# Kernel optimization log

Measured on AMD Instinct MI355X. Metric: run time of the kernel, lower is better.

## Reference

```python
import jax, jax.numpy as jnp
import numpy as np

N_NODES = 100000

def _sage_conv(x, src, dst, W_l, b_l, W_r):
    # PyG SAGEConv(aggr='mean'): out = lin_l(mean_{j in N(i)} x_j) + lin_r(x_i)
    agg = jax.ops.segment_sum(x[src], dst, num_segments=N_NODES)          # [N, F]
    cnt = jax.ops.segment_sum(jnp.ones_like(dst, dtype=x.dtype), dst,
                              num_segments=N_NODES)                        # [N]
    mean = agg / jnp.maximum(cnt, 1.0)[:, None]
    return mean @ W_l + b_l + x @ W_r

def setup_inputs() -> dict:
    key = jax.random.key(0)
    ks = jax.random.split(key, 10)
    F_in, H = 128, 16
    E, P = 1600000, 2000000
    x = jax.random.normal(ks[0], (N_NODES, F_in), dtype=jnp.float32)
    edge_index = jax.random.randint(ks[1], (2, E), 0, N_NODES, dtype=jnp.int64)
    decode_index = jax.random.randint(ks[2], (2, P), 0, N_NODES, dtype=jnp.int64)
    s1 = 1.0 / np.sqrt(F_in)
    s2 = 1.0 / np.sqrt(H)
    W1l = jax.random.uniform(ks[3], (F_in, H), jnp.float32, -s1, s1)
    b1 = jax.random.uniform(ks[4], (H,), jnp.float32, -s1, s1)
    W1r = jax.random.uniform(ks[5], (F_in, H), jnp.float32, -s1, s1)
    W2l = jax.random.uniform(ks[6], (H, H), jnp.float32, -s2, s2)
    b2 = jax.random.uniform(ks[7], (H,), jnp.float32, -s2, s2)
    W2r = jax.random.uniform(ks[8], (H, H), jnp.float32, -s2, s2)
    return {"x": x, "W1l": W1l, "b1": b1, "W1r": W1r,
            "W2l": W2l, "b2": b2, "W2r": W2r,
            "edge_index": edge_index, "decode_index": decode_index}

def reference(x, W1l, b1, W1r, W2l, b2, W2r, edge_index, decode_index):
    src, dst = edge_index[0], edge_index[1]
    h = _sage_conv(x, src, dst, W1l, b1, W1r)          # conv1
    h = jax.nn.relu(h)                                  # relu (dropout: eval -> identity)
    h = _sage_conv(h, src, dst, W2l, b2, W2r)           # conv2
    logits = jnp.sum(h[decode_index[0]] * h[decode_index[1]], axis=1)  # [P]
    return jax.nn.sigmoid(logits)
```

## Files before the change

### kernel.cpp

```cpp
#include <hip/hip_runtime.h>
#include <hip/hip_fp16.h>

#define N_NODES 100000
#define F_IN 128
#define H 16
#define NBIN 391
#define BINCAP 4608
#define ECHUNK 8192
#define QSCALE 4096.0f
#define QINV (1.0f / 4096.0f)

__device__ inline unsigned int packi16(float a, float b) {
  int ia = __float2int_rn(fminf(fmaxf(a * QSCALE, -32767.f), 32767.f));
  int ib = __float2int_rn(fminf(fmaxf(b * QSCALE, -32767.f), 32767.f));
  return (unsigned int)((ia & 0xffff) | (ib << 16));
}

__global__ void __launch_bounds__(512) k_init(int* __restrict__ binCur) {
  int t = threadIdx.x;
  if (t < NBIN) binCur[t] = t * BINCAP;
}

__global__ void __launch_bounds__(256) k_lin1(
    const float* __restrict__ x, const float* __restrict__ W1l,
    const float* __restrict__ W1r, unsigned short* __restrict__ y1l,
    float* __restrict__ y1r) {
  __shared__ float red[3 * 32 * 64];
  int t = threadIdx.x;
  int part = __builtin_amdgcn_readfirstlane(t >> 6);
  int ln = t & 63;
  int n = blockIdx.x * 64 + ln;
  int nc = (n < N_NODES) ? n : (N_NODES - 1);
  const float4* xr = (const float4*)(x + (size_t)nc * F_IN + part * (F_IN / 4));
  float4 xv[8];
#pragma unroll
  for (int j = 0; j < 8; ++j) xv[j] = xr[j];
  const float* Wl = W1l + part * (F_IN / 4) * H;
  const float* Wr = W1r + part * (F_IN / 4) * H;
  float al[H], ar[H];
#pragma unroll
  for (int c = 0; c < H; ++c) { al[c] = 0.f; ar[c] = 0.f; }
#pragma unroll
  for (int j = 0; j < 8; ++j) {
    float xs[4] = {xv[j].x, xv[j].y, xv[j].z, xv[j].w};
#pragma unroll
    for (int jj = 0; jj < 4; ++jj) {
      int k = j * 4 + jj;
#pragma unroll
      for (int c = 0; c < H; ++c) {
        al[c] = fmaf(xs[jj], Wl[k * H + c], al[c]);
        ar[c] = fmaf(xs[jj], Wr[k * H + c], ar[c]);
      }
    }
  }
  if (part != 0) {
    int base = (part - 1) * 2048;
#pragma unroll
    for (int c = 0; c < H; ++c) {
      red[base + c * 64 + ln] = al[c];
      red[base + (H + c) * 64 + ln] = ar[c];
    }
  }
  __syncthreads();
  if (part == 0 && n < N_NODES) {
#pragma unroll
    for (int c = 0; c < H; ++c) {
      al[c] = ((al[c] + red[c * 64 + ln]) + red[2048 + c * 64 + ln])
              + red[4096 + c * 64 + ln];
      ar[c] = ((ar[c] + red[(H + c) * 64 + ln]) + red[2048 + (H + c) * 64 + ln])
              + red[4096 + (H + c) * 64 + ln];
    }
    uint4 w0, w1;
    w0.x = packi16(al[0], al[1]);  w0.y = packi16(al[2], al[3]);
    w0.z = packi16(al[4], al[5]);  w0.w = packi16(al[6], al[7]);
    w1.x = packi16(al[8], al[9]);  w1.y = packi16(al[10], al[11]);
    w1.z = packi16(al[12], al[13]); w1.w = packi16(al[14], al[15]);
    uint4* ol = (uint4*)(y1l + (size_t)n * H);
    ol[0] = w0;
    ol[1] = w1;
    float4* orr = (float4*)(y1r + (size_t)n * H);
#pragma unroll
    for (int q = 0; q < 4; ++q)
      orr[q] = make_float4(ar[4 * q], ar[4 * q + 1], ar[4 * q + 2], ar[4 * q + 3]);
  }
}

__global__ void __launch_bounds__(512) k_binfill(
    const int* __restrict__ src, const int* __restrict__ dst,
    int* __restrict__ binCur, int* __restrict__ recs, int E) {
  __shared__ int hist[512];
  __shared__ int gbase[512];
  __shared__ int cnt2[512];
  int t = threadIdx.x;
  hist[t] = 0;
  cnt2[t] = 0;
  __syncthreads();
  int base = blockIdx.x * ECHUNK;
  int rec[16], bin[16];
#pragma unroll
  for (int j = 0; j < 16; ++j) {
    int e = base + j * 512 + t;
    if (e < E) {
      int s = src[e];
      int d = dst[e];
      rec[j] = (s << 8) | (d & 255);
      bin[j] = d >> 8;
      atomicAdd(&hist[bin[j]], 1);
    } else {
      bin[j] = -1;
    }
  }
  __syncthreads();
  if (t < NBIN) {
    int c = hist[t];
    gbase[t] = (c > 0) ? atomicAdd(&binCur[t], c) : 0;
  }
  __syncthreads();
#pragma unroll
  for (int j = 0; j < 16; ++j) {
    if (bin[j] >= 0) {
      int loc = atomicAdd(&cnt2[bin[j]], 1);
      int slot = gbase[bin[j]] + loc;
      if (slot < (bin[j] + 1) * BINCAP)
        recs[slot] = rec[j];
    }
  }
}

__global__ void __launch_bounds__(512) k_group(
    int* __restrict__ recs, const int* __restrict__ binCur,
    int* __restrict__ deg, int* __restrict__ rowBeg) {
  __shared__ int lrec[BINCAP];
  __shared__ int hist[256];
  __shared__ int off[256];
  __shared__ int cur[256];
  int t = threadIdx.x;
  int b = blockIdx.x;
  int rbase = b * BINCAP;
  int R = binCur[b] - rbase;
  if (R > BINCAP) R = BINCAP;
  if (t < 256) hist[t] = 0;
  __syncthreads();
#pragma unroll
  for (int j = 0; j < 9; ++j) {
    int idx = j * 512 + t;
    if (idx < R) {
      int r = recs[rbase + idx];
      lrec[idx] = r;
      atomicAdd(&hist[r & 255], 1);
    }
  }
  __syncthreads();
  if (t < 256) off[t] = hist[t];
  __syncthreads();
  for (int o = 1; o < 256; o <<= 1) {
    int u = 0;
    if (t < 256 && t >= o) u = off[t - o];
    __syncthreads();
    if (t < 256) off[t] += u;
    __syncthreads();
  }
  if (t < 256) {
    int ex = off[t] - hist[t];
    cur[t] = ex;
    int n = (b << 8) + t;
    if (n < N_NODES) {
      deg[n] = hist[t];
      rowBeg[n] = rbase + ex;
    }
  }
  __syncthreads();
#pragma unroll
  for (int j = 0; j < 9; ++j) {
    int idx = j * 512 + t;
    if (idx < R) {
      int r = lrec[idx];
      int slot = atomicAdd(&cur[r & 255], 1);
      recs[rbase + slot] = r >> 8;
    }
  }
}

__global__ void __launch_bounds__(256) k_gather1(
    const int* __restrict__ srcSorted, const int* __restrict__ deg,
    const int* __restrict__ rowBeg, const unsigned short* __restrict__ y1l,
    const float* __restrict__ y1r, const float* __restrict__ b1,
    const float* __restrict__ W2l, const float* __restrict__ W2r,
    unsigned short* __restrict__ z2l, float* __restrict__ z2r) {
  int tid = blockIdx.x * 256 + threadIdx.x;
  int n = tid >> 2;
  int q = tid & 3;
  if (n >= N_NODES) return;
  int beg = rowBeg[n];
  int dg = deg[n];
  int end = beg + dg;
  int acc0 = 0, acc1 = 0, acc2 = 0, acc3 = 0;
  int i = beg;
  for (; i + 8 <= end; i += 8) {
    int sqa = srcSorted[i + q];
    int sqb = srcSorted[i + 4 + q];
#pragma unroll
    for (int j = 0; j < 4; ++j) {
      int sa = __shfl(sqa, j, 4);
      int sb = __shfl(sqb, j, 4);
      uint2 va = *(const uint2*)(y1l + (size_t)sa * H + q * 4);
      uint2 vb = *(const uint2*)(y1l + (size_t)sb * H + q * 4);
      acc0 += (((int)(va.x << 16)) >> 16) + (((int)(vb.x << 16)) >> 16);
      acc1 += (((int)va.x) >> 16) + (((int)vb.x) >> 16);
      acc2 += (((int)(va.y << 16)) >> 16) + (((int)(vb.y << 16)) >> 16);
      acc3 += (((int)va.y) >> 16) + (((int)vb.y) >> 16);
    }
  }
  for (; i + 4 <= end; i += 4) {
    int sq = srcSorted[i + q];
#pragma unroll
    for (int j = 0; j < 4; ++j) {
      int sj = __shfl(sq, j, 4);
      uint2 v = *(const uint2*)(y1l + (size_t)sj * H + q * 4);
      acc0 += ((int)(v.x << 16)) >> 16;
      acc1 += ((int)v.x) >> 16;
      acc2 += ((int)(v.y << 16)) >> 16;
      acc3 += ((int)v.y) >> 16;
    }
  }
  for (; i < end; ++i) {
    int sj = srcSorted[i];
    uint2 v = *(const uint2*)(y1l + (size_t)sj * H + q * 4);
    acc0 += ((int)(v.x << 16)) >> 16;
    acc1 += ((int)v.x) >> 16;
    acc2 += ((int)(v.y << 16)) >> 16;
    acc3 += ((int)v.y) >> 16;
  }
  float s = (1.f / fmaxf((float)dg, 1.f)) * QINV;
  float4 yr = *(const float4*)(y1r + (size_t)n * H + q * 4);
  float4 bb = *(const float4*)(b1 + q * 4);
  float h1x = fmaxf(fmaf((float)acc0, s, bb.x + yr.x), 0.f);
  float h1y = fmaxf(fmaf((float)acc1, s, bb.y + yr.y), 0.f);
  float h1z = fmaxf(fmaf((float)acc2, s, bb.z + yr.z), 0.f);
  float h1w = fmaxf(fmaf((float)acc3, s, bb.w + yr.w), 0.f);
  float zl0 = 0.f, zl1 = 0.f, zl2 = 0.f, zl3 = 0.f;
  float zr0 = 0.f, zr1 = 0.f, zr2 = 0.f, zr3 = 0.f;
#pragma unroll
  for (int sl = 0; sl < 4; ++sl) {
    float hx = __shfl(h1x, sl, 4);
    float hy = __shfl(h1y, sl, 4);
    float hz = __shfl(h1z, sl, 4);
    float hw = __shfl(h1w, sl, 4);
    float hk4[4] = {hx, hy, hz, hw};
#pragma unroll
    for (int j = 0; j < 4; ++j) {
      int k = sl * 4 + j;
      float4 wl = *(const float4*)(W2l + k * H + q * 4);
      float4 wr = *(const float4*)(W2r + k * H + q * 4);
      float hk = hk4[j];
      zl0 = fmaf(hk, wl.x, zl0); zl1 = fmaf(hk, wl.y, zl1);
      zl2 = fmaf(hk, wl.z, zl2); zl3 = fmaf(hk, wl.w, zl3);
      zr0 = fmaf(hk, wr.x, zr0); zr1 = fmaf(hk, wr.y, zr1);
      zr2 = fmaf(hk, wr.z, zr2); zr3 = fmaf(hk, wr.w, zr3);
    }
  }
  uint2 pk;
  pk.x = packi16(zl0, zl1);
  pk.y = packi16(zl2, zl3);
  *(uint2*)(z2l + (size_t)n * H + q * 4) = pk;
  *(float4*)(z2r + (size_t)n * H + q * 4) = make_float4(zr0, zr1, zr2, zr3);
}

__global__ void __launch_bounds__(256) k_gather2(
    const int* __restrict__ srcSorted, const int* __restrict__ deg,
    const int* __restrict__ rowBeg, const unsigned short* __restrict__ z2l,
    const float* __restrict__ z2r, const float* __restrict__ b2,
    __half* __restrict__ h2) {
  int tid = blockIdx.x * 256 + threadIdx.x;
  int n = tid >> 2;
  int q = tid & 3;
  if (n >= N_NODES) return;
  int beg = rowBeg[n];
  int dg = deg[n];
  int end = beg + dg;
  int acc0 = 0, acc1 = 0, acc2 = 0, acc3 = 0;
  int i = beg;
  for (; i + 8 <= end; i += 8) {
    int sqa = srcSorted[i + q];
    int sqb = srcSorted[i + 4 + q];
#pragma unroll
    for (int j = 0; j < 4; ++j) {
      int sa = __shfl(sqa, j, 4);
      int sb = __shfl(sqb, j, 4);
      uint2 va = *(const uint2*)(z2l + (size_t)sa * H + q * 4);
      uint2 vb = *(const uint2*)(z2l + (size_t)sb * H + q * 4);
      acc0 += (((int)(va.x << 16)) >> 16) + (((int)(vb.x << 16)) >> 16);
      acc1 += (((int)va.x) >> 16) + (((int)vb.x) >> 16);
      acc2 += (((int)(va.y << 16)) >> 16) + (((int)(vb.y << 16)) >> 16);
      acc3 += (((int)va.y) >> 16) + (((int)vb.y) >> 16);
    }
  }
  for (; i + 4 <= end; i += 4) {
    int sq = srcSorted[i + q];
#pragma unroll
    for (int j = 0; j < 4; ++j) {
      int sj = __shfl(sq, j, 4);
      uint2 v = *(const uint2*)(z2l + (size_t)sj * H + q * 4);
      acc0 += ((int)(v.x << 16)) >> 16;
      acc1 += ((int)v.x) >> 16;
      acc2 += ((int)(v.y << 16)) >> 16;
      acc3 += ((int)v.y) >> 16;
    }
  }
  for (; i < end; ++i) {
    int sj = srcSorted[i];
    uint2 v = *(const uint2*)(z2l + (size_t)sj * H + q * 4);
    acc0 += ((int)(v.x << 16)) >> 16;
    acc1 += ((int)v.x) >> 16;
    acc2 += ((int)(v.y << 16)) >> 16;
    acc3 += ((int)v.y) >> 16;
  }
  float s = (1.f / fmaxf((float)dg, 1.f)) * QINV;
  float4 zr = *(const float4*)(z2r + (size_t)n * H + q * 4);
  float4 bb = *(const float4*)(b2 + q * 4);
  float v0 = fmaf((float)acc0, s, bb.x + zr.x);
  float v1 = fmaf((float)acc1, s, bb.y + zr.y);
  float v2 = fmaf((float)acc2, s, bb.z + zr.z);
  float v3 = fmaf((float)acc3, s, bb.w + zr.w);
  __half2 h0 = __floats2half2_rn(v0, v1);
  __half2 h1 = __floats2half2_rn(v2, v3);
  uint2 pk;
  pk.x = *(unsigned int*)&h0;
  pk.y = *(unsigned int*)&h1;
  *(uint2*)(h2 + (size_t)n * H + q * 4) = pk;
}

__device__ inline float dot8h(uint4 u, uint4 v) {
  float acc = 0.f;
  const unsigned int* uw = (const unsigned int*)&u;
  const unsigned int* vw = (const unsigned int*)&v;
#pragma unroll
  for (int j = 0; j < 4; ++j) {
    float2 a = __half22float2(*(const __half2*)&uw[j]);
    float2 b = __half22float2(*(const __half2*)&vw[j]);
    acc = fmaf(a.x, b.x, acc);
    acc = fmaf(a.y, b.y, acc);
  }
  return acc;
}

__global__ void __launch_bounds__(256) k_decode(
    const int* __restrict__ ps, const int* __restrict__ pd,
    const __half* __restrict__ h2, float* __restrict__ out, int P) {
  int t = blockIdx.x * 256 + threadIdx.x;
  int p = t * 2;
  if (p >= P) return;
  int2 av = *(const int2*)(ps + p);
  int2 bv = *(const int2*)(pd + p);
  const uint4* ha0 = (const uint4*)(h2 + (size_t)av.x * H);
  const uint4* hb0 = (const uint4*)(h2 + (size_t)bv.x * H);
  const uint4* ha1 = (const uint4*)(h2 + (size_t)av.y * H);
  const uint4* hb1 = (const uint4*)(h2 + (size_t)bv.y * H);
  uint4 u00 = ha0[0], u01 = ha0[1];
  uint4 v00 = hb0[0], v01 = hb0[1];
  uint4 u10 = ha1[0], u11 = ha1[1];
  uint4 v10 = hb1[0], v11 = hb1[1];
  float d0 = dot8h(u00, v00) + dot8h(u01, v01);
  float d1 = dot8h(u10, v10) + dot8h(u11, v11);
  float o0 = 1.f / (1.f + __expf(-d0));
  float o1 = 1.f / (1.f + __expf(-d1));
  if (p + 1 < P) {
    *(float2*)(out + p) = make_float2(o0, o1);
  } else {
    out[p] = o0;
  }
}

extern "C" void kernel_launch(void* const* d_in, const int* in_sizes, int n_in,
                              void* d_out, int out_size, void* d_ws, size_t ws_size,
                              hipStream_t stream) {
  const float* x   = (const float*)d_in[0];
  const float* W1l = (const float*)d_in[1];
  const float* b1  = (const float*)d_in[2];
  const float* W1r = (const float*)d_in[3];
  const float* W2l = (const float*)d_in[4];
  const float* b2  = (const float*)d_in[5];
  const float* W2r = (const float*)d_in[6];
  const int* ei = (const int*)d_in[7];
  const int* di = (const int*)d_in[8];
  const int E = in_sizes[7] / 2;
  const int P = in_sizes[8] / 2;

  const size_t NF = (size_t)N_NODES * H;
  unsigned short* y1l = (unsigned short*)d_ws;
  __half*         h2  = (__half*)y1l;
  unsigned short* z2l = y1l + NF;
  float*  y1r = (float*)(z2l + NF);
  float*  z2r = y1r;
  int* recs   = (int*)(y1r + NF);
  int* binCur = recs + (size_t)NBIN * BINCAP;
  int* deg    = binCur + 512;
  int* rowBeg = deg + N_NODES;

  const int lin1Blocks = (N_NODES + 63) / 64;
  const int fillBlocks = (E + ECHUNK - 1) / ECHUNK;
  const int gatherBlocks = ((N_NODES * 4) + 255) / 256;
  const int decodeBlocks = ((P + 1) / 2 + 255) / 256;

  k_init<<<1, 512, 0, stream>>>(binCur);
  k_lin1<<<lin1Blocks, 256, 0, stream>>>(x, W1l, W1r, y1l, y1r);
  k_binfill<<<fillBlocks, 512, 0, stream>>>(ei, ei + E, binCur, recs, E);
  k_group<<<NBIN, 512, 0, stream>>>(recs, binCur, deg, rowBeg);
  k_gather1<<<gatherBlocks, 256, 0, stream>>>(recs, deg, rowBeg, y1l, y1r,
                                              b1, W2l, W2r, z2l, z2r);
  k_gather2<<<gatherBlocks, 256, 0, stream>>>(recs, deg, rowBeg, z2l, z2r,
                                              b2, h2);
  k_decode<<<decodeBlocks, 256, 0, stream>>>(di, di + P, h2, (float*)d_out, P);
}
```

Before: 214.6 us.

## Replace CSR grouping and gathers with per-bin shared-memory atomic aggregation

Drops the k_group sorting pass and the per-node CSR gather kernels. Each 256-node bin block now reads its unsorted edge records directly, gathers the 16-channel quantized source rows and accumulates them with LDS integer atomics, then applies the epilogue (mean, bias, relu, second-layer matmul). This removes one kernel launch, the deg/rowBeg arrays and the recs rewrite pass. In exchange there is heavy LDS atomic contention and only 391 blocks, which may underfill the GPU.

```diff
diff --git a/kernel.cpp b/kernel.cpp
--- a/kernel.cpp
+++ b/kernel.cpp
@@ -9,6 +9,9 @@
 #define ECHUNK 8192
 #define QSCALE 4096.0f
 #define QINV (1.0f / 4096.0f)
+
+#define SXL(u) (((int)((u) << 16)) >> 16)
+#define SXH(u) (((int)(u)) >> 16)
 
 __device__ inline unsigned int packi16(float a, float b) {
   int ia = __float2int_rn(fminf(fmaxf(a * QSCALE, -32767.f), 32767.f));
@@ -127,207 +130,178 @@
   }
 }
 
-__global__ void __launch_bounds__(512) k_group(
-    int* __restrict__ recs, const int* __restrict__ binCur,
-    int* __restrict__ deg, int* __restrict__ rowBeg) {
-  __shared__ int lrec[BINCAP];
-  __shared__ int hist[256];
-  __shared__ int off[256];
-  __shared__ int cur[256];
+__global__ void __launch_bounds__(512) k_agg1(
+    const int* __restrict__ recs, const int* __restrict__ binCur,
+    const unsigned short* __restrict__ y1l, const float* __restrict__ y1r,
+    const float* __restrict__ b1, const float* __restrict__ W2l,
+    const float* __restrict__ W2r, unsigned short* __restrict__ z2l,
+    float* __restrict__ z2r) {
+  __shared__ int acc[16][256];
+  __shared__ int cnt[256];
+  __shared__ float hf[16][256];
+  __shared__ float w2l[256];
+  __shared__ float w2r[256];
   int t = threadIdx.x;
   int b = blockIdx.x;
+#pragma unroll
+  for (int j = 0; j < 8; ++j) ((int*)acc)[j * 512 + t] = 0;
+  if (t < 256) { cnt[t] = 0; w2l[t] = W2l[t]; }
+  else         w2r[t - 256] = W2r[t - 256];
+  __syncthreads();
   int rbase = b * BINCAP;
   int R = binCur[b] - rbase;
   if (R > BINCAP) R = BINCAP;
-  if (t < 256) hist[t] = 0;
-  __syncthreads();
+  int rr[9];
 #pragma unroll
   for (int j = 0; j < 9; ++j) {
     int idx = j * 512 + t;
-    if (idx < R) {
-      int r = recs[rbase + idx];
-      lrec[idx] = r;
-      atomicAdd(&hist[r & 255], 1);
-    }
-  }
-  __syncthreads();
-  if (t < 256) off[t] = hist[t];
-  __syncthreads();
-  for (int o = 1; o < 256; o <<= 1) {
-    int u = 0;
-    if (t < 256 && t >= o) u = off[t - o];
-    __syncthreads();
-    if (t < 256) off[t] += u;
-    __syncthreads();
-  }
-  if (t < 256) {
-    int ex = off[t] - hist[t];
-    cur[t] = ex;
-    int n = (b << 8) + t;
-    if (n < N_NODES) {
-      deg[n] = hist[t];
-      rowBeg[n] = rbase + ex;
-    }
-  }
-  __syncthreads();
+    rr[j] = (idx < R) ? recs[rbase + idx] : -1;
+  }
+  uint4 va[9], vb[9];
+#pragma unroll
+  for (int j = 0; j < 9; ++j) {
+    int s = (rr[j] >= 0) ? (rr[j] >> 8) : 0;
+    const uint4* yp = (const uint4*)(y1l + (size_t)s * H);
+    va[j] = yp[0];
+    vb[j] = yp[1];
+  }
+#pragma unroll
+  for (int j = 0; j < 9; ++j) {
+    if (rr[j] >= 0) {
+      int nb = rr[j] & 255;
+      uint4 v0 = va[j], v1 = vb[j];
+      atomicAdd(&cnt[nb], 1);
+      atomicAdd(&acc[0][nb],  SXL(v0.x)); atomicAdd(&acc[1][nb],  SXH(v0.x));
+      atomicAdd(&acc[2][nb],  SXL(v0.y)); atomicAdd(&acc[3][nb],  SXH(v0.y));
+      atomicAdd(&acc[4][nb],  SXL(v0.z)); atomicAdd(&acc[5][nb],  SXH(v0.z));
+      atomicAdd(&acc[6][nb],  SXL(v0.w)); atomicAdd(&acc[7][nb],  SXH(v0.w));
+      atomicAdd(&acc[8][nb],  SXL(v1.x)); atomicAdd(&acc[9][nb],  SXH(v1.x));
+      atomicAdd(&acc[10][nb], SXL(v1.y)); atomicAdd(&acc[11][nb], SXH(v1.y));
+      atomicAdd(&acc[12][nb], SXL(v1.z)); atomicAdd(&acc[13][nb], SXH(v1.z));
+      atomicAdd(&acc[14][nb], SXL(v1.w)); atomicAdd(&acc[15][nb], SXH(v1.w));
+    }
+  }
+  __syncthreads();
+  int node = t >> 1;
+  int half = t & 1;
+  int coff = half * 8;
+  int n = (b << 8) + node;
+  if (n < N_NODES) {
+    float s = QINV / fmaxf((float)cnt[node], 1.f);
+    const float4* yrp = (const float4*)(y1r + (size_t)n * H + coff);
+    float4 y0 = yrp[0], y1v = yrp[1];
+    const float4* bp = (const float4*)(b1 + coff);
+    float4 b0 = bp[0], b1v = bp[1];
+    float yv[8] = {y0.x, y0.y, y0.z, y0.w, y1v.x, y1v.y, y1v.z, y1v.w};
+    float bv[8] = {b0.x, b0.y, b0.z, b0.w, b1v.x, b1v.y, b1v.z, b1v.w};
+#pragma unroll
+    for (int c = 0; c < 8; ++c) {
+      float h = fmaf((float)acc[coff + c][node], s, bv[c] + yv[c]);
+      hf[coff + c][node] = fmaxf(h, 0.f);
+    }
+  } else {
+#pragma unroll
+    for (int c = 0; c < 8; ++c) hf[coff + c][node] = 0.f;
+  }
+  __syncthreads();
+  float zl[8], zr[8];
+#pragma unroll
+  for (int c = 0; c < 8; ++c) { zl[c] = 0.f; zr[c] = 0.f; }
+#pragma unroll
+  for (int k = 0; k < 16; ++k) {
+    float hk = hf[k][node];
+#pragma unroll
+    for (int c = 0; c < 8; ++c) {
+      zl[c] = fmaf(hk, w2l[k * 16 + coff + c], zl[c]);
+      zr[c] = fmaf(hk, w2r[k * 16 + coff + c], zr[c]);
+    }
+  }
+  if (n < N_NODES) {
+    uint4 pk;
+    pk.x = packi16(zl[0], zl[1]);
+    pk.y = packi16(zl[2], zl[3]);
+    pk.z = packi16(zl[4], zl[5]);
+    pk.w = packi16(zl[6], zl[7]);
+    *(uint4*)(z2l + (size_t)n * H + coff) = pk;
+    float4* zp = (float4*)(z2r + (size_t)n * H + coff);
+    zp[0] = make_float4(zr[0], zr[1], zr[2], zr[3]);
+    zp[1] = make_float4(zr[4], zr[5], zr[6], zr[7]);
+  }
+}
+
+__global__ void __launch_bounds__(512) k_agg2(
+    const int* __restrict__ recs, const int* __restrict__ binCur,
+    const unsigned short* __restrict__ z2l, const float* __restrict__ z2r,
+    const float* __restrict__ b2, __half* __restrict__ h2) {
+  __shared__ int acc[16][256];
+  __shared__ int cnt[256];
+  int t = threadIdx.x;
+  int b = blockIdx.x;
+#pragma unroll
+  for (int j = 0; j < 8; ++j) ((int*)acc)[j * 512 + t] = 0;
+  if (t < 256) cnt[t] = 0;
+  __syncthreads();
+  int rbase = b * BINCAP;
+  int R = binCur[b] - rbase;
+  if (R > BINCAP) R = BINCAP;
+  int rr[9];
 #pragma unroll
   for (int j = 0; j < 9; ++j) {
     int idx = j * 512 + t;
-    if (idx < R) {
-      int r = lrec[idx];
-      int slot = atomicAdd(&cur[r & 255], 1);
-      recs[rbase + slot] = r >> 8;
-    }
-  }
-}
-
-__global__ void __launch_bounds__(256) k_gather1(
-    const int* __restrict__ srcSorted, const int* __restrict__ deg,
-    const int* __restrict__ rowBeg, const unsigned short* __restrict__ y1l,
-    const float* __restrict__ y1r, const float* __restrict__ b1,
-    const float* __restrict__ W2l, const float* __restrict__ W2r,
-    unsigned short* __restrict__ z2l, float* __restrict__ z2r) {
-  int tid = blockIdx.x * 256 + threadIdx.x;
-  int n = tid >> 2;
-  int q = tid & 3;
-  if (n >= N_NODES) return;
-  int beg = rowBeg[n];
-  int dg = deg[n];
-  int end = beg + dg;
-  int acc0 = 0, acc1 = 0, acc2 = 0, acc3 = 0;
-  int i = beg;
-  for (; i + 8 <= end; i += 8) {
-    int sqa = srcSorted[i + q];
-    int sqb = srcSorted[i + 4 + q];
-#pragma unroll
-    for (int j = 0; j < 4; ++j) {
-      int sa = __shfl(sqa, j, 4);
-      int sb = __shfl(sqb, j, 4);
-      uint2 va = *(const uint2*)(y1l + (size_t)sa * H + q * 4);
-      uint2 vb = *(const uint2*)(y1l + (size_t)sb * H + q * 4);
-      acc0 += (((int)(va.x << 16)) >> 16) + (((int)(vb.x << 16)) >> 16);
-      acc1 += (((int)va.x) >> 16) + (((int)vb.x) >> 16);
-      acc2 += (((int)(va.y << 16)) >> 16) + (((int)(vb.y << 16)) >> 16);
-      acc3 += (((int)va.y) >> 16) + (((int)vb.y) >> 16);
-    }
-  }
-  for (; i + 4 <= end; i += 4) {
-    int sq = srcSorted[i + q];
-#pragma unroll
-    for (int j = 0; j < 4; ++j) {
-      int sj = __shfl(sq, j, 4);
-      uint2 v = *(const uint2*)(y1l + (size_t)sj * H + q * 4);
-      acc0 += ((int)(v.x << 16)) >> 16;
-      acc1 += ((int)v.x) >> 16;
-      acc2 += ((int)(v.y << 16)) >> 16;
-      acc3 += ((int)v.y) >> 16;
-    }
-  }
-  for (; i < end; ++i) {
-    int sj = srcSorted[i];
-    uint2 v = *(const uint2*)(y1l + (size_t)sj * H + q * 4);
-    acc0 += ((int)(v.x << 16)) >> 16;
-    acc1 += ((int)v.x) >> 16;
-    acc2 += ((int)(v.y << 16)) >> 16;
-    acc3 += ((int)v.y) >> 16;
-  }
-  float s = (1.f / fmaxf((float)dg, 1.f)) * QINV;
-  float4 yr = *(const float4*)(y1r + (size_t)n * H + q * 4);
-  float4 bb = *(const float4*)(b1 + q * 4);
-  float h1x = fmaxf(fmaf((float)acc0, s, bb.x + yr.x), 0.f);
-  float h1y = fmaxf(fmaf((float)acc1, s, bb.y + yr.y), 0.f);
-  float h1z = fmaxf(fmaf((float)acc2, s, bb.z + yr.z), 0.f);
-  float h1w = fmaxf(fmaf((float)acc3, s, bb.w + yr.w), 0.f);
-  float zl0 = 0.f, zl1 = 0.f, zl2 = 0.f, zl3 = 0.f;
-  float zr0 = 0.f, zr1 = 0.f, zr2 = 0.f, zr3 = 0.f;
-#pragma unroll
-  for (int sl = 0; sl < 4; ++sl) {
-    float hx = __shfl(h1x, sl, 4);
-    float hy = __shfl(h1y, sl, 4);
-    float hz = __shfl(h1z, sl, 4);
-    float hw = __shfl(h1w, sl, 4);
-    float hk4[4] = {hx, hy, hz, hw};
-#pragma unroll
-    for (int j = 0; j < 4; ++j) {
-      int k = sl * 4 + j;
-      float4 wl = *(const float4*)(W2l + k * H + q * 4);
-      float4 wr = *(const float4*)(W2r + k * H + q * 4);
-      float hk = hk4[j];
-      zl0 = fmaf(hk, wl.x, zl0); zl1 = fmaf(hk, wl.y, zl1);
-      zl2 = fmaf(hk, wl.z, zl2); zl3 = fmaf(hk, wl.w, zl3);
-      zr0 = fmaf(hk, wr.x, zr0); zr1 = fmaf(hk, wr.y, zr1);
-      zr2 = fmaf(hk, wr.z, zr2); zr3 = fmaf(hk, wr.w, zr3);
-    }
-  }
-  uint2 pk;
-  pk.x = packi16(zl0, zl1);
-  pk.y = packi16(zl2, zl3);
-  *(uint2*)(z2l + (size_t)n * H + q * 4) = pk;
-  *(float4*)(z2r + (size_t)n * H + q * 4) = make_float4(zr0, zr1, zr2, zr3);
-}
-
-__global__ void __launch_bounds__(256) k_gather2(
-    const int* __restrict__ srcSorted, const int* __restrict__ deg,
-    const int* __restrict__ rowBeg, const unsigned short* __restrict__ z2l,
-    const float* __restrict__ z2r, const float* __restrict__ b2,
-    __half* __restrict__ h2) {
-  int tid = blockIdx.x * 256 + threadIdx.x;
-  int n = tid >> 2;
-  int q = tid & 3;
-  if (n >= N_NODES) return;
-  int beg = rowBeg[n];
-  int dg = deg[n];
-  int end = beg + dg;
-  int acc0 = 0, acc1 = 0, acc2 = 0, acc3 = 0;
-  int i = beg;
-  for (; i + 8 <= end; i += 8) {
-    int sqa = srcSorted[i + q];
-    int sqb = srcSorted[i + 4 + q];
-#pragma unroll
-    for (int j = 0; j < 4; ++j) {
-      int sa = __shfl(sqa, j, 4);
-      int sb = __shfl(sqb, j, 4);
-      uint2 va = *(const uint2*)(z2l + (size_t)sa * H + q * 4);
-      uint2 vb = *(const uint2*)(z2l + (size_t)sb * H + q * 4);
-      acc0 += (((int)(va.x << 16)) >> 16) + (((int)(vb.x << 16)) >> 16);
-      acc1 += (((int)va.x) >> 16) + (((int)vb.x) >> 16);
-      acc2 += (((int)(va.y << 16)) >> 16) + (((int)(vb.y << 16)) >> 16);
-      acc3 += (((int)va.y) >> 16) + (((int)vb.y) >> 16);
-    }
-  }
-  for (; i + 4 <= end; i += 4) {
-    int sq = srcSorted[i + q];
-#pragma unroll
-    for (int j = 0; j < 4; ++j) {
-      int sj = __shfl(sq, j, 4);
-      uint2 v = *(const uint2*)(z2l + (size_t)sj * H + q * 4);
-      acc0 += ((int)(v.x << 16)) >> 16;
-      acc1 += ((int)v.x) >> 16;
-      acc2 += ((int)(v.y << 16)) >> 16;
-      acc3 += ((int)v.y) >> 16;
-    }
-  }
-  for (; i < end; ++i) {
-    int sj = srcSorted[i];
-    uint2 v = *(const uint2*)(z2l + (size_t)sj * H + q * 4);
-    acc0 += ((int)(v.x << 16)) >> 16;
-    acc1 += ((int)v.x) >> 16;
-    acc2 += ((int)(v.y << 16)) >> 16;
-    acc3 += ((int)v.y) >> 16;
-  }
-  float s = (1.f / fmaxf((float)dg, 1.f)) * QINV;
-  float4 zr = *(const float4*)(z2r + (size_t)n * H + q * 4);
-  float4 bb = *(const float4*)(b2 + q * 4);
-  float v0 = fmaf((float)acc0, s, bb.x + zr.x);
-  float v1 = fmaf((float)acc1, s, bb.y + zr.y);
-  float v2 = fmaf((float)acc2, s, bb.z + zr.z);
-  float v3 = fmaf((float)acc3, s, bb.w + zr.w);
-  __half2 h0 = __floats2half2_rn(v0, v1);
-  __half2 h1 = __floats2half2_rn(v2, v3);
-  uint2 pk;
-  pk.x = *(unsigned int*)&h0;
-  pk.y = *(unsigned int*)&h1;
-  *(uint2*)(h2 + (size_t)n * H + q * 4) = pk;
+    rr[j] = (idx < R) ? recs[rbase + idx] : -1;
+  }
+  uint4 va[9], vb[9];
+#pragma unroll
+  for (int j = 0; j < 9; ++j) {
+    int s = (rr[j] >= 0) ? (rr[j] >> 8) : 0;
+    const uint4* yp = (const uint4*)(z2l + (size_t)s * H);
+    va[j] = yp[0];
+    vb[j] = yp[1];
+  }
+#pragma unroll
+  for (int j = 0; j < 9; ++j) {
+    if (rr[j] >= 0) {
+      int nb = rr[j] & 255;
+      uint4 v0 = va[j], v1 = vb[j];
+      atomicAdd(&cnt[nb], 1);
+      atomicAdd(&acc[0][nb],  SXL(v0.x)); atomicAdd(&acc[1][nb],  SXH(v0.x));
+      atomicAdd(&acc[2][nb],  SXL(v0.y)); atomicAdd(&acc[3][nb],  SXH(v0.y));
+      atomicAdd(&acc[4][nb],  SXL(v0.z)); atomicAdd(&acc[5][nb],  SXH(v0.z));
+      atomicAdd(&acc[6][nb],  SXL(v0.w)); atomicAdd(&acc[7][nb],  SXH(v0.w));
+      atomicAdd(&acc[8][nb],  SXL(v1.x)); atomicAdd(&acc[9][nb],  SXH(v1.x));
+      atomicAdd(&acc[10][nb], SXL(v1.y)); atomicAdd(&acc[11][nb], SXH(v1.y));
+      atomicAdd(&acc[12][nb], SXL(v1.z)); atomicAdd(&acc[13][nb], SXH(v1.z));
+      atomicAdd(&acc[14][nb], SXL(v1.w)); atomicAdd(&acc[15][nb], SXH(v1.w));
+    }
+  }
+  __syncthreads();
+  int node = t >> 1;
+  int half = t & 1;
+  int coff = half * 8;
+  int n = (b << 8) + node;
+  if (n < N_NODES) {
+    float s = QINV / fmaxf((float)cnt[node], 1.f);
+    const float4* zrp = (const float4*)(z2r + (size_t)n * H + coff);
+    float4 z0 = zrp[0], z1 = zrp[1];
+    const float4* bp = (const float4*)(b2 + coff);
+    float4 b0 = bp[0], b1v = bp[1];
+    float zv[8] = {z0.x, z0.y, z0.z, z0.w, z1.x, z1.y, z1.z, z1.w};
+    float bv[8] = {b0.x, b0.y, b0.z, b0.w, b1v.x, b1v.y, b1v.z, b1v.w};
+    float v[8];
+#pragma unroll
+    for (int c = 0; c < 8; ++c)
+      v[c] = fmaf((float)acc[coff + c][node], s, bv[c] + zv[c]);
+    __half2 h0 = __floats2half2_rn(v[0], v[1]);
+    __half2 h1 = __floats2half2_rn(v[2], v[3]);
+    __half2 h2p = __floats2half2_rn(v[4], v[5]);
+    __half2 h3 = __floats2half2_rn(v[6], v[7]);
+    uint4 pk;
+    pk.x = *(unsigned int*)&h0;
+    pk.y = *(unsigned int*)&h1;
+    pk.z = *(unsigned int*)&h2p;
+    pk.w = *(unsigned int*)&h3;
+    *(uint4*)(h2 + (size_t)n * H + coff) = pk;
+  }
 }
 
 __device__ inline float dot8h(uint4 u, uint4 v) {
@@ -394,21 +368,16 @@
   float*  z2r = y1r;
   int* recs   = (int*)(y1r + NF);
   int* binCur = recs + (size_t)NBIN * BINCAP;
-  int* deg    = binCur + 512;
-  int* rowBeg = deg + N_NODES;
 
   const int lin1Blocks = (N_NODES + 63) / 64;
   const int fillBlocks = (E + ECHUNK - 1) / ECHUNK;
-  const int gatherBlocks = ((N_NODES * 4) + 255) / 256;
   const int decodeBlocks = ((P + 1) / 2 + 255) / 256;
 
   k_init<<<1, 512, 0, stream>>>(binCur);
   k_lin1<<<lin1Blocks, 256, 0, stream>>>(x, W1l, W1r, y1l, y1r);
   k_binfill<<<fillBlocks, 512, 0, stream>>>(ei, ei + E, binCur, recs, E);
-  k_group<<<NBIN, 512, 0, stream>>>(recs, binCur, deg, rowBeg);
-  k_gather1<<<gatherBlocks, 256, 0, stream>>>(recs, deg, rowBeg, y1l, y1r,
-                                              b1, W2l, W2r, z2l, z2r);
-  k_gather2<<<gatherBlocks, 256, 0, stream>>>(recs, deg, rowBeg, z2l, z2r,
-                                              b2, h2);
+  k_agg1<<<NBIN, 512, 0, stream>>>(recs, binCur, y1l, y1r, b1, W2l, W2r,
+                                   z2l, z2r);
+  k_agg2<<<NBIN, 512, 0, stream>>>(recs, binCur, z2l, z2r, b2, h2);
   k_decode<<<decodeBlocks, 256, 0, stream>>>(di, di + P, h2, (float*)d_out, P);
 }
```

After: 207.1 us. 1.04x faster.
